# Kernel optimization log

Hardware: AMD Instinct MI355X
Metric: run time of the kernel (lower is better)

Reference implementation:

```python
import jax, jax.numpy as jnp
import numpy as np

B, N, DIM = 2, 2048, 1024
HEADS, DIM_HEAD = 16, 64
SOFTCAP = 50.0
ROPE_THETA = 10000.0


def setup_inputs() -> dict:
    key = jax.random.key(0)
    k1, k2, k3 = jax.random.split(key, 3)
    x = jax.random.normal(k1, (B, N, DIM), jnp.float32)
    # structured modality positions: (type, offset, length), non-overlapping, in-bounds
    mods = np.zeros((B, 4, 3), np.int64)
    base_offsets = [200, 700, 1200, 1700]
    for b in range(B):
        for m, o in enumerate(base_offsets):
            mods[b, m] = (0, o + b * 16, 256)
    modalities = jnp.asarray(mods)
    gamma = jnp.zeros((DIM,), jnp.float32)           # RMSNorm gamma (init zeros, used as gamma+1)
    w_qkv = jax.random.normal(k2, (DIM, 3 * HEADS * DIM_HEAD), jnp.float32) * 0.02
    w_out = jax.random.normal(k3, (HEADS * DIM_HEAD, DIM), jnp.float32) * 0.02
    return {"x": x, "modalities": modalities, "gamma": gamma, "w_qkv": w_qkv, "w_out": w_out}


def _rotate_half(x):
    # interleaved-pair rotation, matching rotary-embedding-torch default
    x1, x2 = x[..., 0::2], x[..., 1::2]
    return jnp.stack((-x2, x1), axis=-1).reshape(x.shape)


def reference(x, modalities, gamma, w_qkv, w_out):
    b, n, d = x.shape
    h, dh = HEADS, DIM_HEAD
    seq = jnp.arange(n)
    off = modalities[..., 1]      # [b, m]
    length = modalities[..., 2]   # [b, m]

    # --- modality-aware rotary positions (span interior shrunk by offset [1, -1]) ---
    in_span = (seq[None, None, :] >= (off + 1)[:, :, None]) & (seq[None, None, :] < (off + length)[:, :, None])
    is_any_modality = in_span.any(axis=1)                                   # [b, n]
    pos = (seq[None, :] - jnp.cumsum(is_any_modality.astype(jnp.int32), axis=-1)).astype(jnp.float32)

    # --- RMSNorm: l2norm(x) * sqrt(d) * (gamma + 1) ---
    norm = jnp.maximum(jnp.sqrt(jnp.sum(x * x, axis=-1, keepdims=True)), 1e-12)
    xn = x / norm * jnp.sqrt(jnp.float32(d)) * (gamma + 1.0)

    # --- qkv projection, split heads -> [b, h, n, dh] ---
    qkv = (xn @ w_qkv).reshape(b, n, 3, h, dh)
    q, k, v = jnp.moveaxis(qkv, 2, 0)        # each [b, n, h, dh]
    q = jnp.transpose(q, (0, 2, 1, 3))
    k = jnp.transpose(k, (0, 2, 1, 3))
    v = jnp.transpose(v, (0, 2, 1, 3))

    # --- rotary embedding with modality-aware positions ---
    inv_freq = ROPE_THETA ** (-jnp.arange(0, dh, 2, dtype=jnp.float32) / dh)  # [dh/2]
    ang = pos[:, None, :, None] * inv_freq                                    # [b, 1, n, dh/2]
    ang = jnp.repeat(ang, 2, axis=-1)                                         # [b, 1, n, dh]
    cos, sin = jnp.cos(ang), jnp.sin(ang)
    q = q * cos + _rotate_half(q) * sin
    k = k * cos + _rotate_half(k) * sin

    # --- transfusion attention mask: causal OR per-modality bidirectional span ---
    causal_mask = seq[:, None] >= seq[None, :]                                 # [n, n]
    q_ge = seq[None, None, :] >= off[:, :, None]                               # [b, m, n]
    kv_lt = seq[None, None, :] < (off + length)[:, :, None]                    # [b, m, n]
    mod_mask = (q_ge[:, :, :, None] & kv_lt[:, :, None, :]).any(axis=1)        # [b, n, n]
    mask = causal_mask[None] | mod_mask                                        # [b, n, n]

    # --- attention with softclamp(50) ---
    scale = dh ** -0.5
    sim = jnp.einsum('bhid,bhjd->bhij', q, k) * scale
    sim = jnp.tanh(sim / SOFTCAP) * SOFTCAP
    sim = jnp.where(mask[:, None], sim, jnp.finfo(sim.dtype).min)
    attn = jax.nn.softmax(sim, axis=-1)
    out = jnp.einsum('bhij,bhjd->bhid', attn, v)                               # [b, h, n, dh]
    out = jnp.transpose(out, (0, 2, 1, 3)).reshape(b, n, h * dh)
    return out @ w_out
```

## Files before the change

### kernel.cpp

```cpp
#include <hip/hip_runtime.h>
#include <hip/hip_bf16.h>
#include <stdint.h>

#define B_ 2
#define N_ 2048
#define H_ 16
#define DIM_ 1024
#define NH3 3072
#define ROWS (B_*N_)

typedef __attribute__((ext_vector_type(8))) short bf16x8;
typedef __attribute__((ext_vector_type(4))) float f32x4;
typedef unsigned short u16;

__device__ __forceinline__ u16 f2bf(float f){
  union { float f; uint32_t u; } v; v.f = f;
  return (u16)((v.u + 0x7fffu + ((v.u >> 16) & 1u)) >> 16);
}

#if __has_builtin(__builtin_amdgcn_exp2f)
#define EXP2F(x) __builtin_amdgcn_exp2f(x)
#else
#define EXP2F(x) __expf((x) * 0.6931471805599453f)
#endif
#if __has_builtin(__builtin_amdgcn_rcpf)
#define RCPF(x) __builtin_amdgcn_rcpf(x)
#else
#define RCPF(x) (1.0f / (x))
#endif

#define GLL16(g, l) __builtin_amdgcn_global_load_lds( \
    (const __attribute__((address_space(1))) void*)(g), \
    (__attribute__((address_space(3))) void*)(l), 16, 0, 0)

__global__ void k_pos(const int* __restrict__ mods, float* __restrict__ pos){
  const int b = blockIdx.x;
  const int lane = threadIdx.x;
  int off[4], len[4];
#pragma unroll
  for (int m = 0; m < 4; ++m){
    off[m] = mods[(b*4 + m)*3 + 1];
    len[m] = mods[(b*4 + m)*3 + 2];
  }
  int run = 0;
  for (int c = 0; c < N_/64; ++c){
    int n = c*64 + lane;
    int v = 0;
#pragma unroll
    for (int m = 0; m < 4; ++m)
      if (n >= off[m] + 1 && n < off[m] + len[m]) v = 1;
    int s = v;
#pragma unroll
    for (int d = 1; d < 64; d <<= 1){
      int t = __shfl_up(s, d);
      if (lane >= d) s += t;
    }
    pos[b*N_ + n] = (float)(n - (run + s));
    run += __shfl(s, 63);
  }
}

__global__ void k_ropetab(const float* __restrict__ pos, float* __restrict__ cosT, float* __restrict__ sinT){
  int t = blockIdx.x*256 + threadIdx.x;
  if (t >= B_*N_*32) return;
  int f = t & 31, bn = t >> 5;
  float inv = powf(10000.0f, -(float)(2*f) / 64.0f);
  float ang = pos[bn] * inv;
  float s, c;
  sincosf(ang, &s, &c);
  cosT[t] = c; sinT[t] = s;
}

__global__ void k_transpose2(const float* __restrict__ wqkv, const float* __restrict__ wout,
                             u16* __restrict__ wqkvT, u16* __restrict__ woutT){
  __shared__ float tile[32][33];
  const int bx = blockIdx.x;
  const float* src; u16* dst; int C, bc;
  if (bx < 96){ src = wqkv; dst = wqkvT; C = NH3;  bc = bx*32; }
  else        { src = wout; dst = woutT; C = DIM_; bc = (bx-96)*32; }
  const int R = DIM_;
  int tx = threadIdx.x & 31, ty = threadIdx.x >> 5;
  int br = blockIdx.y * 32;
#pragma unroll
  for (int i = 0; i < 32; i += 8)
    tile[ty + i][tx] = src[(size_t)(br + ty + i)*C + bc + tx];
  __syncthreads();
#pragma unroll
  for (int i = 0; i < 32; i += 8)
    dst[(size_t)(bc + ty + i)*R + br + tx] = f2bf(tile[tx][ty + i]);
}

__global__ __launch_bounds__(256) void k_rmsnorm(const float* __restrict__ x, const float* __restrict__ gamma, u16* __restrict__ xn){
  int row = blockIdx.x, t = threadIdx.x;
  const float4 xv = ((const float4*)(x + (size_t)row*DIM_))[t];
  float ss = xv.x*xv.x + xv.y*xv.y + xv.z*xv.z + xv.w*xv.w;
#pragma unroll
  for (int d = 1; d < 64; d <<= 1) ss += __shfl_xor(ss, d);
  __shared__ float red[4];
  if ((t & 63) == 0) red[t >> 6] = ss;
  __syncthreads();
  float tot = red[0] + red[1] + red[2] + red[3];
  float scl = 32.0f / fmaxf(sqrtf(tot), 1e-12f);
  const float4 gv = ((const float4*)gamma)[t];
  ushort4 o;
  o.x = f2bf(xv.x * scl * (gv.x + 1.0f));
  o.y = f2bf(xv.y * scl * (gv.y + 1.0f));
  o.z = f2bf(xv.z * scl * (gv.z + 1.0f));
  o.w = f2bf(xv.w * scl * (gv.w + 1.0f));
  ((ushort4*)(xn + (size_t)row*DIM_))[t] = o;
}

template<int MODE, int BM>
__global__ __launch_bounds__(256) void k_gemm(
    const u16* __restrict__ A, const u16* __restrict__ Bt,
    int K, int Nc,
    float* __restrict__ outf,
    const float* __restrict__ cosT, const float* __restrict__ sinT,
    u16* __restrict__ qo, u16* __restrict__ ko, u16* __restrict__ vt)
{
  constexpr int MR = BM/32;
  constexpr int RA = BM/8;
  constexpr int CNT = (RA + 16)/4;
  __shared__ u16 lA[BM*64];
  __shared__ u16 lB[128*64];
  const int tid = threadIdx.x;
  const int wid = tid >> 6, lane = tid & 63;
  const int nx = gridDim.x;
  const int orig = blockIdx.y * nx + blockIdx.x;
  const int qq = (nx * gridDim.y) >> 3;
  const int wgid = (orig & 7) * qq + (orig >> 3);
  const int m0 = (wgid % nx) * BM, n0 = (wgid / nx) * 128;
  const int wm = wid >> 1, wn = wid & 1;
  const int srow = lane >> 3, sch = lane & 7;
  const int r16 = lane & 15, g4 = lane >> 4;
  f32x4 acc[MR][4] = {};
  const int ksteps = K >> 6;
  for (int kt = 0; kt < ksteps; ++kt){
    const int kb = kt*64;
    const int gch = sch ^ srow;
#pragma unroll
    for (int i = 0; i < CNT; ++i){
      const int reg = wid*CNT + i;
      if (reg < RA){
        const int row = reg*8 + srow;
        GLL16(A + (size_t)(m0 + row)*K + kb + gch*8, &lA[reg*512]);
      } else {
        const int r2 = reg - RA;
        const int row = r2*8 + srow;
        GLL16(Bt + (size_t)(n0 + row)*K + kb + gch*8, &lB[r2*512]);
      }
    }
    __syncthreads();
#pragma unroll
    for (int t = 0; t < 2; ++t){
      bf16x8 af[MR], bfr[4];
#pragma unroll
      for (int m = 0; m < MR; ++m){
        int row = wm*(BM/2) + m*16 + r16;
        int ch = (t*4 + g4) ^ (r16 & 7);
        af[m] = *(const bf16x8*)&lA[row*64 + ch*8];
      }
#pragma unroll
      for (int n = 0; n < 4; ++n){
        int row = wn*64 + n*16 + r16;
        int ch = (t*4 + g4) ^ (r16 & 7);
        bfr[n] = *(const bf16x8*)&lB[row*64 + ch*8];
      }
#pragma unroll
      for (int m = 0; m < MR; ++m)
#pragma unroll
        for (int n = 0; n < 4; ++n)
          acc[m][n] = __builtin_amdgcn_mfma_f32_16x16x32_bf16(af[m], bfr[n], acc[m][n], 0, 0, 0);
    }
    __syncthreads();
  }
#pragma unroll
  for (int m = 0; m < MR; ++m){
#pragma unroll
    for (int n = 0; n < 4; ++n){
      if constexpr (MODE == 0){
        const int gcol = n0 + wn*64 + n*16 + r16;
        const int s3 = gcol >> 10, hh = (gcol >> 6) & 15, d = gcol & 63;
        const int grow0 = m0 + wm*(BM/2) + m*16 + g4*4;
        const int b = grow0 >> 11, nn0 = grow0 & (N_-1);
        const size_t hb = (size_t)(b*H_ + hh);
        if (s3 == 2){
          uint32_t w01, w23;
          asm("v_cvt_pk_bf16_f32 %0, %1, %2" : "=v"(w01) : "v"(acc[m][n][0]), "v"(acc[m][n][1]));
          asm("v_cvt_pk_bf16_f32 %0, %1, %2" : "=v"(w23) : "v"(acc[m][n][2]), "v"(acc[m][n][3]));
          *reinterpret_cast<uint2*>(&vt[(hb*64 + d)*N_ + nn0]) = make_uint2(w01, w23);
        } else {
#pragma unroll
          for (int r = 0; r < 4; ++r){
            const float v = acc[m][n][r];
            const float part = __shfl_xor(v, 1);
            const int nn = nn0 + r;
            const int pidx = (b*N_ + nn)*32 + (d >> 1);
            const float c = cosT[pidx], sn = sinT[pidx];
            const float rot = (d & 1) ? (v*c + part*sn) : (v*c - part*sn);
            const u16 val = f2bf(rot);
            if (s3 == 0) qo[(hb*N_ + nn)*64 + d] = val;
            else         ko[(hb*N_ + nn)*64 + d] = val;
          }
        }
      } else {
#pragma unroll
        for (int r = 0; r < 4; ++r){
          const int grow = m0 + wm*(BM/2) + m*16 + g4*4 + r;
          const int gcol = n0 + wn*64 + n*16 + r16;
          outf[(size_t)grow*Nc + gcol] = acc[m][n][r];
        }
      }
    }
  }
}

#define PST 68
__global__ __launch_bounds__(256) void k_attn(
    const u16* __restrict__ qb, const u16* __restrict__ kb, const u16* __restrict__ vt,
    const int* __restrict__ mods, u16* __restrict__ xo)
{
  __shared__ u16 lK[64*64];
  __shared__ u16 lV[64*64];
  __shared__ u16 lP[4*16*PST];
  const int tid = threadIdx.x, wid = tid >> 6, lane = tid & 63;
  const int id = blockIdx.x;
  const int xcd = id & 7, rank = id >> 3;
  const int bh = xcd + 8*(rank & 3);
  const int qt = 31 - (rank >> 2);
  const int b = bh >> 4, h = bh & 15;
  const int r16 = lane & 15, g4 = lane >> 4;
  const int srow = lane >> 3, sch = lane & 7;
  int moff[4], mend[4];
#pragma unroll
  for (int m = 0; m < 4; ++m){
    moff[m] = mods[(b*4+m)*3+1];
    mend[m] = moff[m] + mods[(b*4+m)*3+2];
  }
  const u16* kbase = kb + (size_t)bh*N_*64;
  const u16* vbase = vt + (size_t)bh*64*N_;
  u16* lPw = &lP[wid*16*PST];

  const int q0 = qt*64 + wid*16;
  const int i  = q0 + r16;
  const int imax = qt*64 + 63;
  int jmax = 0;
#pragma unroll
  for (int m = 0; m < 4; ++m)
    if (i >= moff[m]) jmax = max(jmax, mend[m]);
  const u16* qrow = qb + ((size_t)bh*N_ + q0 + r16)*64;
  const bf16x8 aq0 = *(const bf16x8*)&qrow[g4*8];
  const bf16x8 aq1 = *(const bf16x8*)&qrow[32 + g4*8];
  f32x4 o[4] = {};
  f32x4 acc_s = {};
  bf16x8 ones;
#pragma unroll
  for (int j = 0; j < 8; ++j) ones[j] = (short)0x3F80;

  const float D1 = 0.18033688011112043f;
  const float D3 = -3.7570183356483704e-07f;
  const float D5 = 9.392544618418597e-13f;

  for (int kt = 0; kt < N_/64; ++kt){
    bool proc = (kt*64 <= imax);
    if (!proc){
#pragma unroll
      for (int m = 0; m < 4; ++m)
        if (imax >= moff[m] && kt*64 < mend[m]) proc = true;
    }
    if (!proc) continue;
    __syncthreads();
#pragma unroll
    for (int ld = 0; ld < 2; ++ld){
      int reg = wid*2 + ld;
      int row = reg*8 + srow;
      int gch = sch ^ srow;
      GLL16(kbase + (size_t)(kt*64 + row)*64 + gch*8, &lK[reg*512]);
      GLL16(vbase + (size_t)row*N_ + kt*64 + gch*8,   &lV[reg*512]);
    }
    __syncthreads();
    f32x4 s[4] = {};
    __builtin_amdgcn_s_setprio(1);
#pragma unroll
    for (int cb = 0; cb < 4; ++cb){
#pragma unroll
      for (int t = 0; t < 2; ++t){
        int row = cb*16 + r16;
        int ch = (t*4 + g4) ^ (row & 7);
        bf16x8 bk = *(const bf16x8*)&lK[row*64 + ch*8];
        s[cb] = __builtin_amdgcn_mfma_f32_16x16x32_bf16(bk, t ? aq1 : aq0, s[cb], 0, 0, 0);
      }
    }
    __builtin_amdgcn_s_setprio(0);
    const int thr = max(i, jmax - 1) - kt*64;
    const bool nomask = (kt*64 + 63 <= q0);
#pragma unroll
    for (int cb = 0; cb < 4; ++cb){
      float p[4];
#pragma unroll
      for (int r = 0; r < 4; ++r){
        const float sv = s[cb][r];
        const float w = sv*sv;
        p[r] = EXP2F(sv * fmaf(w, fmaf(w, D5, D3), D1));
      }
      if (!nomask){
#pragma unroll
        for (int r = 0; r < 4; ++r)
          p[r] = (cb*16 + g4*4 + r <= thr) ? p[r] : 0.0f;
      }
      uint32_t w01, w23;
      asm("v_cvt_pk_bf16_f32 %0, %1, %2" : "=v"(w01) : "v"(p[0]), "v"(p[1]));
      asm("v_cvt_pk_bf16_f32 %0, %1, %2" : "=v"(w23) : "v"(p[2]), "v"(p[3]));
      *reinterpret_cast<uint2*>(&lPw[r16*PST + cb*16 + g4*4]) = make_uint2(w01, w23);
    }
    asm volatile("s_waitcnt lgkmcnt(0)" ::: "memory");
    __builtin_amdgcn_sched_barrier(0);
    union { uint2 h[2]; bf16x8 v; } u0, u1;
    u0.h[0] = *(const uint2*)&lPw[r16*PST + g4*8];
    u0.h[1] = *(const uint2*)&lPw[r16*PST + g4*8 + 4];
    u1.h[0] = *(const uint2*)&lPw[r16*PST + 32 + g4*8];
    u1.h[1] = *(const uint2*)&lPw[r16*PST + 32 + g4*8 + 4];
    __builtin_amdgcn_s_setprio(1);
    acc_s = __builtin_amdgcn_mfma_f32_16x16x32_bf16(u0.v, ones, acc_s, 0, 0, 0);
    acc_s = __builtin_amdgcn_mfma_f32_16x16x32_bf16(u1.v, ones, acc_s, 0, 0, 0);
#pragma unroll
    for (int cb = 0; cb < 4; ++cb){
#pragma unroll
      for (int t = 0; t < 2; ++t){
        int d = cb*16 + r16;
        int ch = (t*4 + g4) ^ (d & 7);
        bf16x8 bv = *(const bf16x8*)&lV[d*64 + ch*8];
        o[cb] = __builtin_amdgcn_mfma_f32_16x16x32_bf16(t ? u1.v : u0.v, bv, o[cb], 0, 0, 0);
      }
    }
    __builtin_amdgcn_s_setprio(0);
  }
#pragma unroll
  for (int r = 0; r < 4; ++r){
    const float linv = RCPF(acc_s[r]);
    const int iq = q0 + g4*4 + r;
#pragma unroll
    for (int cb = 0; cb < 4; ++cb)
      xo[(size_t)(b*N_ + iq)*DIM_ + h*64 + cb*16 + r16] = f2bf(o[cb][r]*linv);
  }
}

extern "C" void kernel_launch(void* const* d_in, const int* in_sizes, int n_in,
                              void* d_out, int out_size, void* d_ws, size_t ws_size,
                              hipStream_t stream){
  const float* x     = (const float*)d_in[0];
  const int*   mods  = (const int*)d_in[1];
  const float* gamma = (const float*)d_in[2];
  const float* wqkv  = (const float*)d_in[3];
  const float* wout  = (const float*)d_in[4];
  float* outp = (float*)d_out;

  char* p = (char*)d_ws;
  auto alloc = [&](size_t bytes) -> char* {
    char* r = p; p += (bytes + 255) & ~(size_t)255; return r;
  };
  float* pos   = (float*)alloc((size_t)B_*N_*4);
  float* cosT  = (float*)alloc((size_t)B_*N_*32*4);
  float* sinT  = (float*)alloc((size_t)B_*N_*32*4);
  u16* wqkvT   = (u16*)alloc((size_t)NH3*DIM_*2);
  u16* woutT   = (u16*)alloc((size_t)DIM_*DIM_*2);
  u16* xn      = (u16*)alloc((size_t)ROWS*DIM_*2);
  u16* qbb     = (u16*)alloc((size_t)B_*H_*N_*64*2);
  u16* kbb     = (u16*)alloc((size_t)B_*H_*N_*64*2);
  u16* vtb     = (u16*)alloc((size_t)B_*H_*N_*64*2);
  u16* xo      = (u16*)alloc((size_t)ROWS*DIM_*2);

  k_pos<<<B_, 64, 0, stream>>>(mods, pos);
  k_ropetab<<<(B_*N_*32 + 255)/256, 256, 0, stream>>>(pos, cosT, sinT);
  k_transpose2<<<dim3(128, 32), 256, 0, stream>>>(wqkv, wout, wqkvT, woutT);
  k_rmsnorm<<<ROWS, 256, 0, stream>>>(x, gamma, xn);
  k_gemm<0,128><<<dim3(ROWS/128, NH3/128), 256, 0, stream>>>(xn, wqkvT, DIM_, NH3, nullptr, cosT, sinT, qbb, kbb, vtb);
  k_attn<<<1024, 256, 0, stream>>>(qbb, kbb, vtb, mods, xo);
  k_gemm<1,64><<<dim3(ROWS/64, DIM_/128), 256, 0, stream>>>(xo, woutT, DIM_, DIM_, outp, nullptr, nullptr, nullptr, nullptr, nullptr);
}
```

Before: 127.3 us.

## Split attention KV tiles across two blocks and combine partials in a new kernel

Each query tile's key/value tiles are now dealt out alternately to two blocks, so the attention grid doubles from 1024 to 2048 blocks. Each block writes its unnormalized partial output as bf16, along with its partial row sum, to a workspace. A new k_comb kernel adds the two halves, normalizes, and writes the head-interleaved output. This targets load imbalance and low parallelism in long causal rows, at the cost of an extra launch, extra global traffic for the partials, and rounding the partials to bf16 before they are combined.

```diff
diff --git a/kernel.cpp b/kernel.cpp
--- a/kernel.cpp
+++ b/kernel.cpp
@@ -8,6 +8,7 @@
 #define DIM_ 1024
 #define NH3 3072
 #define ROWS (B_*N_)
+#define BHN (B_*H_*N_)
 
 typedef __attribute__((ext_vector_type(8))) short bf16x8;
 typedef __attribute__((ext_vector_type(4))) float f32x4;
@@ -16,6 +17,9 @@
 __device__ __forceinline__ u16 f2bf(float f){
   union { float f; uint32_t u; } v; v.f = f;
   return (u16)((v.u + 0x7fffu + ((v.u >> 16) & 1u)) >> 16);
+}
+__device__ __forceinline__ float bf2f(u16 h){
+  union { uint32_t u; float f; } v; v.u = ((uint32_t)h) << 16; return v.f;
 }
 
 #if __has_builtin(__builtin_amdgcn_exp2f)
@@ -218,7 +222,7 @@
 #define PST 68
 __global__ __launch_bounds__(256) void k_attn(
     const u16* __restrict__ qb, const u16* __restrict__ kb, const u16* __restrict__ vt,
-    const int* __restrict__ mods, u16* __restrict__ xo)
+    const int* __restrict__ mods, u16* __restrict__ po, float* __restrict__ ps)
 {
   __shared__ u16 lK[64*64];
   __shared__ u16 lV[64*64];
@@ -227,8 +231,10 @@
   const int id = blockIdx.x;
   const int xcd = id & 7, rank = id >> 3;
   const int bh = xcd + 8*(rank & 3);
-  const int qt = 31 - (rank >> 2);
-  const int b = bh >> 4, h = bh & 15;
+  const int qh = rank >> 2;
+  const int qt = 31 - (qh >> 1);
+  const int half = qh & 1;
+  const int b = bh >> 4;
   const int r16 = lane & 15, g4 = lane >> 4;
   const int srow = lane >> 3, sch = lane & 7;
   int moff[4], mend[4];
@@ -261,6 +267,7 @@
   const float D3 = -3.7570183356483704e-07f;
   const float D5 = 9.392544618418597e-13f;
 
+  int tcnt = 0;
   for (int kt = 0; kt < N_/64; ++kt){
     bool proc = (kt*64 <= imax);
     if (!proc){
@@ -269,6 +276,9 @@
         if (imax >= moff[m] && kt*64 < mend[m]) proc = true;
     }
     if (!proc) continue;
+    const bool mine = ((tcnt & 1) == half);
+    ++tcnt;
+    if (!mine) continue;
     __syncthreads();
 #pragma unroll
     for (int ld = 0; ld < 2; ++ld){
@@ -335,14 +345,34 @@
     }
     __builtin_amdgcn_s_setprio(0);
   }
+  u16*   pob = po + ((size_t)half*BHN + (size_t)bh*N_)*64;
+  float* psb = ps + (size_t)half*BHN + (size_t)bh*N_;
 #pragma unroll
   for (int r = 0; r < 4; ++r){
-    const float linv = RCPF(acc_s[r]);
     const int iq = q0 + g4*4 + r;
 #pragma unroll
     for (int cb = 0; cb < 4; ++cb)
-      xo[(size_t)(b*N_ + iq)*DIM_ + h*64 + cb*16 + r16] = f2bf(o[cb][r]*linv);
-  }
+      pob[(size_t)iq*64 + cb*16 + r16] = f2bf(o[cb][r]);
+    if (r16 == 0) psb[iq] = acc_s[r];
+  }
+}
+
+__global__ __launch_bounds__(256) void k_comb(const u16* __restrict__ po, const float* __restrict__ ps,
+                                              u16* __restrict__ xo){
+  const int g = blockIdx.x*256 + threadIdx.x;
+  const int row = g >> 4, c4 = g & 15;
+  const size_t off = (size_t)row*64 + c4*4;
+  const ushort4 a = *(const ushort4*)(po + off);
+  const ushort4 c = *(const ushort4*)(po + (size_t)BHN*64 + off);
+  const float linv = RCPF(ps[row] + ps[BHN + row]);
+  const int bh = row >> 11, iq = row & (N_-1);
+  const int b = bh >> 4, h = bh & 15;
+  ushort4 r;
+  r.x = f2bf((bf2f(a.x) + bf2f(c.x)) * linv);
+  r.y = f2bf((bf2f(a.y) + bf2f(c.y)) * linv);
+  r.z = f2bf((bf2f(a.z) + bf2f(c.z)) * linv);
+  r.w = f2bf((bf2f(a.w) + bf2f(c.w)) * linv);
+  *(ushort4*)(xo + ((size_t)(b*N_ + iq))*DIM_ + h*64 + c4*4) = r;
 }
 
 extern "C" void kernel_launch(void* const* d_in, const int* in_sizes, int n_in,
@@ -365,16 +395,19 @@
   u16* wqkvT   = (u16*)alloc((size_t)NH3*DIM_*2);
   u16* woutT   = (u16*)alloc((size_t)DIM_*DIM_*2);
   u16* xn      = (u16*)alloc((size_t)ROWS*DIM_*2);
-  u16* qbb     = (u16*)alloc((size_t)B_*H_*N_*64*2);
-  u16* kbb     = (u16*)alloc((size_t)B_*H_*N_*64*2);
-  u16* vtb     = (u16*)alloc((size_t)B_*H_*N_*64*2);
+  u16* qbb     = (u16*)alloc((size_t)BHN*64*2);
+  u16* kbb     = (u16*)alloc((size_t)BHN*64*2);
+  u16* vtb     = (u16*)alloc((size_t)BHN*64*2);
   u16* xo      = (u16*)alloc((size_t)ROWS*DIM_*2);
+  u16* po      = (u16*)alloc((size_t)2*BHN*64*2);
+  float* ps    = (float*)alloc((size_t)2*BHN*4);
 
   k_pos<<<B_, 64, 0, stream>>>(mods, pos);
   k_ropetab<<<(B_*N_*32 + 255)/256, 256, 0, stream>>>(pos, cosT, sinT);
   k_transpose2<<<dim3(128, 32), 256, 0, stream>>>(wqkv, wout, wqkvT, woutT);
   k_rmsnorm<<<ROWS, 256, 0, stream>>>(x, gamma, xn);
   k_gemm<0,128><<<dim3(ROWS/128, NH3/128), 256, 0, stream>>>(xn, wqkvT, DIM_, NH3, nullptr, cosT, sinT, qbb, kbb, vtb);
-  k_attn<<<1024, 256, 0, stream>>>(qbb, kbb, vtb, mods, xo);
+  k_attn<<<2048, 256, 0, stream>>>(qbb, kbb, vtb, mods, po, ps);
+  k_comb<<<(BHN*16)/256, 256, 0, stream>>>(po, ps, xo);
   k_gemm<1,64><<<dim3(ROWS/64, DIM_/128), 256, 0, stream>>>(xo, woutT, DIM_, DIM_, outp, nullptr, nullptr, nullptr, nullptr, nullptr);
 }
```

New measurement: 137.6 us. +8.1%, slower.
